# Kernel tuning notes

Measured on AMD Instinct MI355X. Metric: run time of the kernel, lower is better.

Reference implementation:

```python
import jax, jax.numpy as jnp
import numpy as np

N, E, H = 50000, 800000, 4
IN_C, HID_C, OUT_C = 128, 64, 40
NEG_SLOPE_ATT = 0.2   # PyG GATConv default
NEG_SLOPE_ACT = 0.1   # model's LeakyReLU
BN_EPS = 1e-5


def setup_inputs() -> dict:
    key = jax.random.key(0)
    ks = jax.random.split(key, 20)
    x = jax.random.normal(ks[0], (N, IN_C), dtype=jnp.float32)
    adj_m = jax.random.randint(ks[1], (2, E), 0, N, dtype=jnp.int64)
    def glorot(k, shape):
        fan = sum(shape[:2]) if len(shape) == 2 else shape[-1] * 2
        return jax.random.normal(k, shape, dtype=jnp.float32) * (2.0 / fan) ** 0.5
    W0  = glorot(ks[2], (IN_C, H * HID_C))
    as0 = glorot(ks[3], (H, HID_C)); ad0 = glorot(ks[4], (H, HID_C))
    b0  = jnp.zeros((H * HID_C,), jnp.float32)
    W1  = glorot(ks[5], (H * HID_C, H * HID_C))
    as1 = glorot(ks[6], (H, HID_C)); ad1 = glorot(ks[7], (H, HID_C))
    b1  = jnp.zeros((H * HID_C,), jnp.float32)
    # layer 2: 256 -> 40, heads averaged (concat=False)
    W2  = glorot(ks[8], (H * HID_C, H * OUT_C))
    as2 = glorot(ks[9], (H, OUT_C)); ad2 = glorot(ks[10], (H, OUT_C))
    b2  = jnp.zeros((OUT_C,), jnp.float32)
    g0 = jnp.ones((H * HID_C,), jnp.float32); be0 = jnp.zeros((H * HID_C,), jnp.float32)
    g1 = jnp.ones((H * HID_C,), jnp.float32); be1 = jnp.zeros((H * HID_C,), jnp.float32)
    return dict(x=x, adj_m=adj_m, W0=W0, as0=as0, ad0=ad0, b0=b0,
                W1=W1, as1=as1, ad1=ad1, b1=b1, W2=W2, as2=as2, ad2=ad2, b2=b2,
                g0=g0, be0=be0, g1=g1, be1=be1)


def gat_conv(x, src, dst, W, att_src, att_dst, bias, concat):
    n = x.shape[0]
    heads, out_c = att_src.shape
    h = (x @ W).reshape(n, heads, out_c)                       # [N,H,C]
    a_src = jnp.einsum('nhc,hc->nh', h, att_src)               # [N,H]
    a_dst = jnp.einsum('nhc,hc->nh', h, att_dst)
    e = jax.nn.leaky_relu(a_src[src] + a_dst[dst], NEG_SLOPE_ATT)  # [E,H]
    # segment softmax over edges grouped by destination node
    m = jax.ops.segment_max(e, dst, num_segments=n)
    m = jnp.where(jnp.isfinite(m), m, 0.0)
    ee = jnp.exp(e - m[dst])
    s = jax.ops.segment_sum(ee, dst, num_segments=n)
    alpha = ee / (s[dst] + 1e-16)                              # [E,H]
    msg = h[src] * alpha[:, :, None]                           # [E,H,C]
    out = jax.ops.segment_sum(msg, dst, num_segments=n)        # [N,H,C]
    if concat:
        return out.reshape(n, heads * out_c) + bias
    return out.mean(axis=1) + bias


def batch_norm(x, gamma, beta):
    mu = x.mean(axis=0)
    var = x.var(axis=0)
    return (x - mu) * jax.lax.rsqrt(var + BN_EPS) * gamma + beta


def reference(x, adj_m, W0, as0, ad0, b0, W1, as1, ad1, b1,
              W2, as2, ad2, b2, g0, be0, g1, be1):
    n = x.shape[0]
    loop = jnp.arange(n, dtype=adj_m.dtype)
    src = jnp.concatenate([adj_m[0], loop])   # add self-loops (PyG default)
    dst = jnp.concatenate([adj_m[1], loop])
    h = gat_conv(x, src, dst, W0, as0, ad0, b0, True)
    h = jax.nn.leaky_relu(batch_norm(h, g0, be0), NEG_SLOPE_ACT)
    h = gat_conv(h, src, dst, W1, as1, ad1, b1, True)
    h = jax.nn.leaky_relu(batch_norm(h, g1, be1), NEG_SLOPE_ACT)
    h = gat_conv(h, src, dst, W2, as2, ad2, b2, False)
    return jax.nn.log_softmax(h, axis=-1)
```

## Files before the change

kernel.cpp:

```cpp
#include <hip/hip_runtime.h>

#define NNODES 50000
#define NEDGES 800000
#define EPTOT  (NEDGES + NNODES)
#define SCAN_NB ((NNODES + 255) / 256)

typedef unsigned short u16;
typedef unsigned int   u32;
typedef __attribute__((ext_vector_type(8))) short s16x8;
typedef __attribute__((ext_vector_type(4))) float f32x4;

static __device__ __forceinline__ float lrelu(float x, float s) { return x > 0.f ? x : s * x; }
static __device__ __forceinline__ float bf2f(u16 b) { return __uint_as_float((u32)b << 16); }
static __device__ __forceinline__ u16 f2bf(float f) {
  u32 u = __float_as_uint(f);
  u32 r = (u + 0x7FFFu + ((u >> 16) & 1u)) >> 16;
  return (u16)r;
}

__device__ __forceinline__ float wred_max(float v) {
#pragma unroll
  for (int off = 32; off; off >>= 1) v = fmaxf(v, __shfl_xor(v, off));
  return v;
}
__device__ __forceinline__ float wred_sum(float v) {
#pragma unroll
  for (int off = 32; off; off >>= 1) v += __shfl_xor(v, off);
  return v;
}

__global__ void k_hist(const int* __restrict__ adj, int* __restrict__ deg) {
  int i = blockIdx.x * blockDim.x + threadIdx.x;
  if (i >= EPTOT) return;
  int d = (i < NEDGES) ? adj[NEDGES + i] : (i - NEDGES);
  atomicAdd(&deg[d], 1);
}

__global__ __launch_bounds__(256) void k_scan1(const int* __restrict__ deg,
                                               int* __restrict__ part,
                                               int* __restrict__ bsum) {
  __shared__ int sm[256];
  int t = threadIdx.x;
  int i = blockIdx.x * 256 + t;
  int v = (i < NNODES) ? deg[i] : 0;
  sm[t] = v;
  __syncthreads();
#pragma unroll
  for (int off = 1; off < 256; off <<= 1) {
    int u = (t >= off) ? sm[t - off] : 0;
    __syncthreads();
    sm[t] += u;
    __syncthreads();
  }
  if (i < NNODES) part[i] = sm[t] - v;
  if (t == 255) bsum[blockIdx.x] = sm[255];
}

__global__ __launch_bounds__(256) void k_scan2(int* __restrict__ bsum) {
  __shared__ int sm[256];
  int t = threadIdx.x;
  int v = (t < SCAN_NB) ? bsum[t] : 0;
  sm[t] = v;
  __syncthreads();
#pragma unroll
  for (int off = 1; off < 256; off <<= 1) {
    int u = (t >= off) ? sm[t - off] : 0;
    __syncthreads();
    sm[t] += u;
    __syncthreads();
  }
  if (t < SCAN_NB) bsum[t] = sm[t] - v;
}

__global__ __launch_bounds__(256) void k_scan3(const int* __restrict__ part,
                                               const int* __restrict__ bsum,
                                               int* __restrict__ rowptr,
                                               int* __restrict__ fill) {
  int i = blockIdx.x * 256 + threadIdx.x;
  if (i == 0) rowptr[NNODES] = EPTOT;
  if (i >= NNODES) return;
  int r = part[i] + bsum[blockIdx.x];
  rowptr[i] = r;
  fill[i] = r;
}

__global__ void k_fill(const int* __restrict__ adj, int* __restrict__ fill,
                       int* __restrict__ colx) {
  int i = blockIdx.x * blockDim.x + threadIdx.x;
  if (i >= EPTOT) return;
  int s, d;
  if (i < NEDGES) { s = adj[i]; d = adj[NEDGES + i]; }
  else            { s = i - NEDGES; d = s; }
  int pos = atomicAdd(&fill[d], 1);
  colx[pos] = s;
}

__global__ void k_wt(const float* __restrict__ W, u16* __restrict__ Wt, int K, int Nc) {
  int i = blockIdx.x * blockDim.x + threadIdx.x;
  if (i >= K * Nc) return;
  int n = i % Nc, k = i / Nc;
  Wt[(size_t)n * K + k] = f2bf(W[i]);
}

__global__ __launch_bounds__(256) void k_gemm_mfma(const float* __restrict__ A,
                                                   const u16* __restrict__ Wt,
                                                   u16* __restrict__ Cb,
                                                   const float* __restrict__ sc,
                                                   const float* __restrict__ sh,
                                                   int M, int K, int Nc) {
  __shared__ u16 As[128 * 40];
  __shared__ u16 Bs[128 * 40];
  const int tid = threadIdx.x;
  const int lane = tid & 63;
  const int wv = tid >> 6;
  const int wr = (wv >> 1) * 64, wc = (wv & 1) * 64;
  const int lr = lane & 15, lk = (lane >> 4) * 8;
  const int bm = blockIdx.x * 128, bn = blockIdx.y * 128;

  const int row0 = tid >> 2, kc0 = (tid & 3) * 8;
  const int ch1 = tid + 256;
  const int row1 = ch1 >> 2, kc1 = (ch1 & 3) * 8;

  f32x4 acc[4][4];
#pragma unroll
  for (int i = 0; i < 4; ++i)
#pragma unroll
    for (int j = 0; j < 4; ++j) {
      f32x4 z = {0.f, 0.f, 0.f, 0.f};
      acc[i][j] = z;
    }

  for (int k0 = 0; k0 < K; k0 += 32) {
    float4 a00 = {0,0,0,0}, a01 = {0,0,0,0}, a10 = {0,0,0,0}, a11 = {0,0,0,0};
    uint4 bv0 = {0,0,0,0}, bv1 = {0,0,0,0};
    {
      int ga = bm + row0;
      if (ga < M) {
        const float* p = A + (size_t)ga * K + k0 + kc0;
        a00 = *(const float4*)p; a01 = *(const float4*)(p + 4);
      }
      int gb = bn + row0;
      if (gb < Nc) bv0 = *(const uint4*)(Wt + (size_t)gb * K + k0 + kc0);
    }
    {
      int ga = bm + row1;
      if (ga < M) {
        const float* p = A + (size_t)ga * K + k0 + kc1;
        a10 = *(const float4*)p; a11 = *(const float4*)(p + 4);
      }
      int gb = bn + row1;
      if (gb < Nc) bv1 = *(const uint4*)(Wt + (size_t)gb * K + k0 + kc1);
    }
    if (sc) {
      const float* s0p = sc + k0 + kc0; const float* h0p = sh + k0 + kc0;
      a00.x = lrelu(fmaf(a00.x, s0p[0], h0p[0]), 0.1f);
      a00.y = lrelu(fmaf(a00.y, s0p[1], h0p[1]), 0.1f);
      a00.z = lrelu(fmaf(a00.z, s0p[2], h0p[2]), 0.1f);
      a00.w = lrelu(fmaf(a00.w, s0p[3], h0p[3]), 0.1f);
      a01.x = lrelu(fmaf(a01.x, s0p[4], h0p[4]), 0.1f);
      a01.y = lrelu(fmaf(a01.y, s0p[5], h0p[5]), 0.1f);
      a01.z = lrelu(fmaf(a01.z, s0p[6], h0p[6]), 0.1f);
      a01.w = lrelu(fmaf(a01.w, s0p[7], h0p[7]), 0.1f);
      const float* s1p = sc + k0 + kc1; const float* h1p = sh + k0 + kc1;
      a10.x = lrelu(fmaf(a10.x, s1p[0], h1p[0]), 0.1f);
      a10.y = lrelu(fmaf(a10.y, s1p[1], h1p[1]), 0.1f);
      a10.z = lrelu(fmaf(a10.z, s1p[2], h1p[2]), 0.1f);
      a10.w = lrelu(fmaf(a10.w, s1p[3], h1p[3]), 0.1f);
      a11.x = lrelu(fmaf(a11.x, s1p[4], h1p[4]), 0.1f);
      a11.y = lrelu(fmaf(a11.y, s1p[5], h1p[5]), 0.1f);
      a11.z = lrelu(fmaf(a11.z, s1p[6], h1p[6]), 0.1f);
      a11.w = lrelu(fmaf(a11.w, s1p[7], h1p[7]), 0.1f);
    }
    ushort4 h00 = {f2bf(a00.x), f2bf(a00.y), f2bf(a00.z), f2bf(a00.w)};
    ushort4 h01 = {f2bf(a01.x), f2bf(a01.y), f2bf(a01.z), f2bf(a01.w)};
    ushort4 h10 = {f2bf(a10.x), f2bf(a10.y), f2bf(a10.z), f2bf(a10.w)};
    ushort4 h11 = {f2bf(a11.x), f2bf(a11.y), f2bf(a11.z), f2bf(a11.w)};

    __syncthreads();
    *(ushort4*)&As[row0 * 40 + kc0]     = h00;
    *(ushort4*)&As[row0 * 40 + kc0 + 4] = h01;
    *(ushort4*)&As[row1 * 40 + kc1]     = h10;
    *(ushort4*)&As[row1 * 40 + kc1 + 4] = h11;
    *(uint4*)&Bs[row0 * 40 + kc0] = bv0;
    *(uint4*)&Bs[row1 * 40 + kc1] = bv1;
    __syncthreads();

    s16x8 af[4], bfm[4];
#pragma unroll
    for (int mi = 0; mi < 4; ++mi)
      af[mi] = *(const s16x8*)&As[(wr + mi * 16 + lr) * 40 + lk];
#pragma unroll
    for (int ni = 0; ni < 4; ++ni)
      bfm[ni] = *(const s16x8*)&Bs[(wc + ni * 16 + lr) * 40 + lk];
#pragma unroll
    for (int mi = 0; mi < 4; ++mi)
#pragma unroll
      for (int ni = 0; ni < 4; ++ni)
        acc[mi][ni] = __builtin_amdgcn_mfma_f32_16x16x32_bf16(af[mi], bfm[ni], acc[mi][ni], 0, 0, 0);
  }

#pragma unroll
  for (int mi = 0; mi < 4; ++mi) {
    int rowb = bm + wr + mi * 16 + (lane >> 4) * 4;
#pragma unroll
    for (int ni = 0; ni < 4; ++ni) {
      int col = bn + wc + ni * 16 + lr;
      if (col >= Nc) continue;
#pragma unroll
      for (int r = 0; r < 4; ++r) {
        int row = rowb + r;
        if (row < M) Cb[(size_t)row * Nc + col] = f2bf(acc[mi][ni][r]);
      }
    }
  }
}

__global__ __launch_bounds__(256) void k_att_hid(const u16* __restrict__ hb,
                                                 const float* __restrict__ asw,
                                                 const float* __restrict__ adw,
                                                 float* __restrict__ asrc,
                                                 float* __restrict__ adst) {
  int wid = blockIdx.x * 4 + (threadIdx.x >> 6);
  int lane = threadIdx.x & 63;
  if (wid >= NNODES) return;
  const u16* hp = hb + (size_t)wid * 256;
  float v0 = bf2f(hp[lane]), v1 = bf2f(hp[64 + lane]);
  float v2 = bf2f(hp[128 + lane]), v3 = bf2f(hp[192 + lane]);
  float ps0 = v0 * asw[lane],       pd0 = v0 * adw[lane];
  float ps1 = v1 * asw[64 + lane],  pd1 = v1 * adw[64 + lane];
  float ps2 = v2 * asw[128 + lane], pd2 = v2 * adw[128 + lane];
  float ps3 = v3 * asw[192 + lane], pd3 = v3 * adw[192 + lane];
  ps0 = wred_sum(ps0); ps1 = wred_sum(ps1); ps2 = wred_sum(ps2); ps3 = wred_sum(ps3);
  pd0 = wred_sum(pd0); pd1 = wred_sum(pd1); pd2 = wred_sum(pd2); pd3 = wred_sum(pd3);
  if (lane == 0) {
    asrc[wid * 4 + 0] = ps0; asrc[wid * 4 + 1] = ps1;
    asrc[wid * 4 + 2] = ps2; asrc[wid * 4 + 3] = ps3;
    adst[wid * 4 + 0] = pd0; adst[wid * 4 + 1] = pd1;
    adst[wid * 4 + 2] = pd2; adst[wid * 4 + 3] = pd3;
  }
}

__global__ __launch_bounds__(256) void k_att_l2(const u16* __restrict__ hb2,
                                                const float* __restrict__ asw,
                                                const float* __restrict__ adw,
                                                float* __restrict__ asrc,
                                                float* __restrict__ adst) {
  int wid = blockIdx.x * 4 + (threadIdx.x >> 6);
  int lane = threadIdx.x & 63;
  if (wid >= NNODES) return;
  const u16* hp = hb2 + (size_t)wid * 160;
  float ps0 = 0, ps1 = 0, ps2 = 0, ps3 = 0, pd0 = 0, pd1 = 0, pd2 = 0, pd3 = 0;
  if (lane < 40) {
    float v0 = bf2f(hp[lane]), v1 = bf2f(hp[40 + lane]);
    float v2 = bf2f(hp[80 + lane]), v3 = bf2f(hp[120 + lane]);
    ps0 = v0 * asw[lane];       pd0 = v0 * adw[lane];
    ps1 = v1 * asw[40 + lane];  pd1 = v1 * adw[40 + lane];
    ps2 = v2 * asw[80 + lane];  pd2 = v2 * adw[80 + lane];
    ps3 = v3 * asw[120 + lane]; pd3 = v3 * adw[120 + lane];
  }
  ps0 = wred_sum(ps0); ps1 = wred_sum(ps1); ps2 = wred_sum(ps2); ps3 = wred_sum(ps3);
  pd0 = wred_sum(pd0); pd1 = wred_sum(pd1); pd2 = wred_sum(pd2); pd3 = wred_sum(pd3);
  if (lane == 0) {
    asrc[wid * 4 + 0] = ps0; asrc[wid * 4 + 1] = ps1;
    asrc[wid * 4 + 2] = ps2; asrc[wid * 4 + 3] = ps3;
    adst[wid * 4 + 0] = pd0; adst[wid * 4 + 1] = pd1;
    adst[wid * 4 + 2] = pd2; adst[wid * 4 + 3] = pd3;
  }
}

__global__ __launch_bounds__(256) void k_aggr_hid(const u16* __restrict__ hb,
                                                  const float* __restrict__ asrc,
                                                  const float* __restrict__ adst,
                                                  const int* __restrict__ rowptr,
                                                  const int* __restrict__ colx,
                                                  const float* __restrict__ bias,
                                                  u16* __restrict__ ew,
                                                  float* __restrict__ out) {
  int wid = blockIdx.x * 4 + (threadIdx.x >> 6);
  int lane = threadIdx.x & 63;
  if (wid >= NNODES) return;
  int beg = rowptr[wid], end = rowptr[wid + 1];
  float ad0 = adst[wid * 4 + 0], ad1 = adst[wid * 4 + 1];
  float ad2 = adst[wid * 4 + 2], ad3 = adst[wid * 4 + 3];

  float s0 = 0.f, s1 = 0.f, s2 = 0.f, s3 = 0.f;
  for (int i = beg + lane; i < end; i += 64) {
    int s = colx[i];
    const float* ap = asrc + (size_t)s * 4;
    float e0 = expf(lrelu(ap[0] + ad0, 0.2f));
    float e1 = expf(lrelu(ap[1] + ad1, 0.2f));
    float e2 = expf(lrelu(ap[2] + ad2, 0.2f));
    float e3 = expf(lrelu(ap[3] + ad3, 0.2f));
    ushort4 w4 = {f2bf(e0), f2bf(e1), f2bf(e2), f2bf(e3)};
    *(ushort4*)(ew + (size_t)i * 4) = w4;
    s0 += e0; s1 += e1; s2 += e2; s3 += e3;
  }
  s0 = wred_sum(s0); s1 = wred_sum(s1); s2 = wred_sum(s2); s3 = wred_sum(s3);

  int q = lane >> 4;
  float sq = (q == 0) ? s0 : (q == 1) ? s1 : (q == 2) ? s2 : s3;

  float ax = 0.f, ay = 0.f, az = 0.f, aw = 0.f;
  const u16* hbl = hb + lane * 4;
  int i = beg;
  for (; i + 4 <= end; i += 4) {
    int e0 = colx[i], e1 = colx[i + 1], e2 = colx[i + 2], e3 = colx[i + 3];
    float w0 = bf2f(ew[(size_t)i * 4 + q]);
    float w1 = bf2f(ew[(size_t)(i + 1) * 4 + q]);
    float w2 = bf2f(ew[(size_t)(i + 2) * 4 + q]);
    float w3 = bf2f(ew[(size_t)(i + 3) * 4 + q]);
    ushort4 r0 = *(const ushort4*)(hbl + (size_t)e0 * 256);
    ushort4 r1 = *(const ushort4*)(hbl + (size_t)e1 * 256);
    ushort4 r2 = *(const ushort4*)(hbl + (size_t)e2 * 256);
    ushort4 r3 = *(const ushort4*)(hbl + (size_t)e3 * 256);
    ax = fmaf(w0, bf2f(r0.x), ax); ay = fmaf(w0, bf2f(r0.y), ay);
    az = fmaf(w0, bf2f(r0.z), az); aw = fmaf(w0, bf2f(r0.w), aw);
    ax = fmaf(w1, bf2f(r1.x), ax); ay = fmaf(w1, bf2f(r1.y), ay);
    az = fmaf(w1, bf2f(r1.z), az); aw = fmaf(w1, bf2f(r1.w), aw);
    ax = fmaf(w2, bf2f(r2.x), ax); ay = fmaf(w2, bf2f(r2.y), ay);
    az = fmaf(w2, bf2f(r2.z), az); aw = fmaf(w2, bf2f(r2.w), aw);
    ax = fmaf(w3, bf2f(r3.x), ax); ay = fmaf(w3, bf2f(r3.y), ay);
    az = fmaf(w3, bf2f(r3.z), az); aw = fmaf(w3, bf2f(r3.w), aw);
  }
  for (; i < end; ++i) {
    int e0 = colx[i];
    float w0 = bf2f(ew[(size_t)i * 4 + q]);
    ushort4 r0 = *(const ushort4*)(hbl + (size_t)e0 * 256);
    ax = fmaf(w0, bf2f(r0.x), ax); ay = fmaf(w0, bf2f(r0.y), ay);
    az = fmaf(w0, bf2f(r0.z), az); aw = fmaf(w0, bf2f(r0.w), aw);
  }
  float inv = 1.f / (sq + 1e-16f);
  float4 b4 = ((const float4*)bias)[lane];
  float4 o = {fmaf(ax, inv, b4.x), fmaf(ay, inv, b4.y),
              fmaf(az, inv, b4.z), fmaf(aw, inv, b4.w)};
  ((float4*)out)[(size_t)wid * 64 + lane] = o;
}

__global__ __launch_bounds__(256) void k_aggr_l2(const u16* __restrict__ hb2,
                                                 const float* __restrict__ asrc,
                                                 const float* __restrict__ adst,
                                                 const int* __restrict__ rowptr,
                                                 const int* __restrict__ colx,
                                                 const float* __restrict__ b2,
                                                 u16* __restrict__ ew,
                                                 float* __restrict__ out) {
  __shared__ float tile[4][160];
  int wv = threadIdx.x >> 6;
  int wid = blockIdx.x * 4 + wv;
  int lane = threadIdx.x & 63;
  bool valid = (wid < NNODES);
  int beg = 0, end = 0;
  float ad0 = 0, ad1 = 0, ad2 = 0, ad3 = 0;
  if (valid) {
    beg = rowptr[wid]; end = rowptr[wid + 1];
    ad0 = adst[wid * 4 + 0]; ad1 = adst[wid * 4 + 1];
    ad2 = adst[wid * 4 + 2]; ad3 = adst[wid * 4 + 3];
  }
  float s0 = 0.f, s1 = 0.f, s2 = 0.f, s3 = 0.f;
  for (int i = beg + lane; i < end; i += 64) {
    int s = colx[i];
    const float* ap = asrc + (size_t)s * 4;
    float e0 = expf(lrelu(ap[0] + ad0, 0.2f));
    float e1 = expf(lrelu(ap[1] + ad1, 0.2f));
    float e2 = expf(lrelu(ap[2] + ad2, 0.2f));
    float e3 = expf(lrelu(ap[3] + ad3, 0.2f));
    ushort4 w4 = {f2bf(e0), f2bf(e1), f2bf(e2), f2bf(e3)};
    *(ushort4*)(ew + (size_t)i * 4) = w4;
    s0 += e0; s1 += e1; s2 += e2; s3 += e3;
  }
  s0 = wred_sum(s0); s1 = wred_sum(s1); s2 = wred_sum(s2); s3 = wred_sum(s3);

  int q = lane / 10; if (q > 3) q = 3;
  float sq = (q == 0) ? s0 : (q == 1) ? s1 : (q == 2) ? s2 : s3;

  float ax = 0.f, ay = 0.f, az = 0.f, aw = 0.f;
  const u16* hbl = hb2 + lane * 4;
  int i = beg;
  for (; i + 4 <= end; i += 4) {
    int e0 = colx[i], e1 = colx[i + 1], e2 = colx[i + 2], e3 = colx[i + 3];
    float w0 = bf2f(ew[(size_t)i * 4 + q]);
    float w1 = bf2f(ew[(size_t)(i + 1) * 4 + q]);
    float w2 = bf2f(ew[(size_t)(i + 2) * 4 + q]);
    float w3 = bf2f(ew[(size_t)(i + 3) * 4 + q]);
    if (lane < 40) {
      ushort4 r0 = *(const ushort4*)(hbl + (size_t)e0 * 160);
      ushort4 r1 = *(const ushort4*)(hbl + (size_t)e1 * 160);
      ushort4 r2 = *(const ushort4*)(hbl + (size_t)e2 * 160);
      ushort4 r3 = *(const ushort4*)(hbl + (size_t)e3 * 160);
      ax = fmaf(w0, bf2f(r0.x), ax); ay = fmaf(w0, bf2f(r0.y), ay);
      az = fmaf(w0, bf2f(r0.z), az); aw = fmaf(w0, bf2f(r0.w), aw);
      ax = fmaf(w1, bf2f(r1.x), ax); ay = fmaf(w1, bf2f(r1.y), ay);
      az = fmaf(w1, bf2f(r1.z), az); aw = fmaf(w1, bf2f(r1.w), aw);
      ax = fmaf(w2, bf2f(r2.x), ax); ay = fmaf(w2, bf2f(r2.y), ay);
      az = fmaf(w2, bf2f(r2.z), az); aw = fmaf(w2, bf2f(r2.w), aw);
      ax = fmaf(w3, bf2f(r3.x), ax); ay = fmaf(w3, bf2f(r3.y), ay);
      az = fmaf(w3, bf2f(r3.z), az); aw = fmaf(w3, bf2f(r3.w), aw);
    }
  }
  for (; i < end; ++i) {
    int e0 = colx[i];
    float w0 = bf2f(ew[(size_t)i * 4 + q]);
    if (lane < 40) {
      ushort4 r0 = *(const ushort4*)(hbl + (size_t)e0 * 160);
      ax = fmaf(w0, bf2f(r0.x), ax); ay = fmaf(w0, bf2f(r0.y), ay);
      az = fmaf(w0, bf2f(r0.z), az); aw = fmaf(w0, bf2f(r0.w), aw);
    }
  }
  if (valid && lane < 40) {
    float inv = 1.f / (sq + 1e-16f);
    tile[wv][lane * 4 + 0] = ax * inv;
    tile[wv][lane * 4 + 1] = ay * inv;
    tile[wv][lane * 4 + 2] = az * inv;
    tile[wv][lane * 4 + 3] = aw * inv;
  }
  __syncthreads();
  int c = lane;
  float val = -3.0e38f;
  if (valid && c < 40) {
    val = 0.25f * (tile[wv][c] + tile[wv][c + 40] + tile[wv][c + 80] + tile[wv][c + 120]) + b2[c];
  }
  float mv = (valid && c < 40) ? val : -3.0e38f;
  mv = wred_max(mv);
  float ex = (valid && c < 40) ? expf(val - mv) : 0.f;
  ex = wred_sum(ex);
  if (valid && c < 40) out[(size_t)wid * 40 + c] = val - mv - logf(ex);
}

__global__ __launch_bounds__(256) void k_bnstats(const float* __restrict__ x,
                                                 float* __restrict__ stat) {
  int c = threadIdx.x;
  const int rows = (NNODES + gridDim.x - 1) / gridDim.x;
  int r0 = blockIdx.x * rows;
  int r1 = min(NNODES, r0 + rows);
  float s = 0.f, qq = 0.f;
  for (int r = r0; r < r1; ++r) {
    float v = x[(size_t)r * 256 + c];
    s += v;
    qq = fmaf(v, v, qq);
  }
  atomicAdd(&stat[c], s);
  atomicAdd(&stat[256 + c], qq);
}

__global__ void k_bnfin(const float* __restrict__ stat, const float* __restrict__ g,
                        const float* __restrict__ be, float* __restrict__ sc,
                        float* __restrict__ sh) {
  int c = threadIdx.x;
  float mean = stat[c] * (1.0f / NNODES);
  float var = stat[256 + c] * (1.0f / NNODES) - mean * mean;
  float inv = rsqrtf(var + 1e-5f);
  float a = g[c] * inv;
  sc[c] = a;
  sh[c] = be[c] - mean * a;
}

extern "C" void kernel_launch(void* const* d_in, const int* in_sizes, int n_in,
                              void* d_out, int out_size, void* d_ws, size_t ws_size,
                              hipStream_t stream) {
  const float* x   = (const float*)d_in[0];
  const int*   adj = (const int*)d_in[1];
  const float* W0  = (const float*)d_in[2];
  const float* as0 = (const float*)d_in[3];
  const float* ad0 = (const float*)d_in[4];
  const float* b0  = (const float*)d_in[5];
  const float* W1  = (const float*)d_in[6];
  const float* as1 = (const float*)d_in[7];
  const float* ad1 = (const float*)d_in[8];
  const float* b1  = (const float*)d_in[9];
  const float* W2  = (const float*)d_in[10];
  const float* as2 = (const float*)d_in[11];
  const float* ad2 = (const float*)d_in[12];
  const float* b2  = (const float*)d_in[13];
  const float* g0  = (const float*)d_in[14];
  const float* be0 = (const float*)d_in[15];
  const float* g1  = (const float*)d_in[16];
  const float* be1 = (const float*)d_in[17];
  float* out = (float*)d_out;

  float* ws   = (float*)d_ws;
  float* bufA = ws;
  float* asrc = bufA + (size_t)NNODES * 256;
  float* adst = asrc + (size_t)NNODES * 4;
  float* stat = adst + (size_t)NNODES * 4;
  float* bnsc = stat + 512;
  float* bnsh = bnsc + 256;
  u16*   hb   = (u16*)(bnsh + 256);
  u16*   w0t  = hb + (size_t)NNODES * 256;
  u16*   w1t  = w0t + 256 * 128;
  u16*   w2t  = w1t + 256 * 256;
  u16*   ew   = w2t + 160 * 256;
  int* rowptr = (int*)(ew + (size_t)EPTOT * 4);
  int* fill   = rowptr + (NNODES + 1);
  int* colx   = fill + NNODES;
  int* deg    = colx + EPTOT;
  int* part   = deg + NNODES;
  int* bsum   = part + NNODES;

  hipMemsetAsync(deg, 0, NNODES * sizeof(int), stream);
  k_hist<<<(EPTOT + 255) / 256, 256, 0, stream>>>(adj, deg);
  k_scan1<<<SCAN_NB, 256, 0, stream>>>(deg, part, bsum);
  k_scan2<<<1, 256, 0, stream>>>(bsum);
  k_scan3<<<SCAN_NB, 256, 0, stream>>>(part, bsum, rowptr, fill);
  k_fill<<<(EPTOT + 255) / 256, 256, 0, stream>>>(adj, fill, colx);

  k_wt<<<(128 * 256 + 255) / 256, 256, 0, stream>>>(W0, w0t, 128, 256);
  k_wt<<<(256 * 256 + 255) / 256, 256, 0, stream>>>(W1, w1t, 256, 256);
  k_wt<<<(256 * 160 + 255) / 256, 256, 0, stream>>>(W2, w2t, 256, 160);

  dim3 gg2((NNODES + 127) / 128, 2);

  k_gemm_mfma<<<gg2, 256, 0, stream>>>(x, w0t, hb, nullptr, nullptr, NNODES, 128, 256);
  k_att_hid<<<12500, 256, 0, stream>>>(hb, as0, ad0, asrc, adst);
  k_aggr_hid<<<12500, 256, 0, stream>>>(hb, asrc, adst, rowptr, colx, b0, ew, bufA);
  hipMemsetAsync(stat, 0, 512 * sizeof(float), stream);
  k_bnstats<<<400, 256, 0, stream>>>(bufA, stat);
  k_bnfin<<<1, 256, 0, stream>>>(stat, g0, be0, bnsc, bnsh);

  k_gemm_mfma<<<gg2, 256, 0, stream>>>(bufA, w1t, hb, bnsc, bnsh, NNODES, 256, 256);
  k_att_hid<<<12500, 256, 0, stream>>>(hb, as1, ad1, asrc, adst);
  k_aggr_hid<<<12500, 256, 0, stream>>>(hb, asrc, adst, rowptr, colx, b1, ew, bufA);
  hipMemsetAsync(stat, 0, 512 * sizeof(float), stream);
  k_bnstats<<<400, 256, 0, stream>>>(bufA, stat);
  k_bnfin<<<1, 256, 0, stream>>>(stat, g1, be1, bnsc, bnsh);

  k_gemm_mfma<<<gg2, 256, 0, stream>>>(bufA, w2t, hb, bnsc, bnsh, NNODES, 256, 160);
  k_att_l2<<<12500, 256, 0, stream>>>(hb, as2, ad2, asrc, adst);
  k_aggr_l2<<<12500, 256, 0, stream>>>(hb, asrc, adst, rowptr, colx, b2, ew, out);
}
```

Before: 575.1 us.

## Fuse attention logits into GEMM epilogue and store hidden activations as bf16

Folds the per-node attention dot products for the hidden layers into the MFMA GEMM epilogue, reducing each 16-lane group with shuffles and accumulating into zeroed asrc/adst buffers with atomics. This removes a separate pass over the GEMM output. Hidden-layer aggregation outputs are also stored as bf16 instead of fp32, which halves traffic for the batch-norm statistics pass and for the next GEMM's A loads. The cost is extra memsets and atomics, plus some precision loss from bf16 intermediates and from the changed order of atomic summation.

```diff
diff --git a/kernel.cpp b/kernel.cpp
--- a/kernel.cpp
+++ b/kernel.cpp
@@ -102,11 +102,49 @@
   Wt[(size_t)n * K + k] = f2bf(W[i]);
 }
 
-__global__ __launch_bounds__(256) void k_gemm_mfma(const float* __restrict__ A,
+template <int ABF>
+__device__ __forceinline__ void load_a_chunk(const void* __restrict__ Av, int ga, int M,
+                                             int K, int koff, const float* __restrict__ sc,
+                                             const float* __restrict__ sh,
+                                             ushort4& lo, ushort4& hi) {
+  float f[8];
+  if (ABF) {
+    uint4 av = {0, 0, 0, 0};
+    if (ga < M) av = *(const uint4*)((const u16*)Av + (size_t)ga * K + koff);
+    u32 w[4] = {av.x, av.y, av.z, av.w};
+#pragma unroll
+    for (int j = 0; j < 4; ++j) {
+      f[2 * j]     = bf2f((u16)(w[j] & 0xffffu));
+      f[2 * j + 1] = bf2f((u16)(w[j] >> 16));
+    }
+  } else {
+    float4 a0 = {0, 0, 0, 0}, a1 = {0, 0, 0, 0};
+    if (ga < M) {
+      const float* p = (const float*)Av + (size_t)ga * K + koff;
+      a0 = *(const float4*)p;
+      a1 = *(const float4*)(p + 4);
+    }
+    f[0] = a0.x; f[1] = a0.y; f[2] = a0.z; f[3] = a0.w;
+    f[4] = a1.x; f[5] = a1.y; f[6] = a1.z; f[7] = a1.w;
+  }
+  if (sc) {
+#pragma unroll
+    for (int j = 0; j < 8; ++j) f[j] = lrelu(fmaf(f[j], sc[koff + j], sh[koff + j]), 0.1f);
+  }
+  lo = (ushort4){f2bf(f[0]), f2bf(f[1]), f2bf(f[2]), f2bf(f[3])};
+  hi = (ushort4){f2bf(f[4]), f2bf(f[5]), f2bf(f[6]), f2bf(f[7])};
+}
+
+template <int ABF, int ATT>
+__global__ __launch_bounds__(256) void k_gemm_mfma(const void* __restrict__ Av,
                                                    const u16* __restrict__ Wt,
                                                    u16* __restrict__ Cb,
                                                    const float* __restrict__ sc,
                                                    const float* __restrict__ sh,
+                                                   const float* __restrict__ asw,
+                                                   const float* __restrict__ adw,
+                                                   float* __restrict__ asrc,
+                                                   float* __restrict__ adst,
                                                    int M, int K, int Nc) {
   __shared__ u16 As[128 * 40];
   __shared__ u16 Bs[128 * 40];
@@ -131,50 +169,12 @@
     }
 
   for (int k0 = 0; k0 < K; k0 += 32) {
-    float4 a00 = {0,0,0,0}, a01 = {0,0,0,0}, a10 = {0,0,0,0}, a11 = {0,0,0,0};
-    uint4 bv0 = {0,0,0,0}, bv1 = {0,0,0,0};
-    {
-      int ga = bm + row0;
-      if (ga < M) {
-        const float* p = A + (size_t)ga * K + k0 + kc0;
-        a00 = *(const float4*)p; a01 = *(const float4*)(p + 4);
-      }
-      int gb = bn + row0;
-      if (gb < Nc) bv0 = *(const uint4*)(Wt + (size_t)gb * K + k0 + kc0);
-    }
-    {
-      int ga = bm + row1;
-      if (ga < M) {
-        const float* p = A + (size_t)ga * K + k0 + kc1;
-        a10 = *(const float4*)p; a11 = *(const float4*)(p + 4);
-      }
-      int gb = bn + row1;
-      if (gb < Nc) bv1 = *(const uint4*)(Wt + (size_t)gb * K + k0 + kc1);
-    }
-    if (sc) {
-      const float* s0p = sc + k0 + kc0; const float* h0p = sh + k0 + kc0;
-      a00.x = lrelu(fmaf(a00.x, s0p[0], h0p[0]), 0.1f);
-      a00.y = lrelu(fmaf(a00.y, s0p[1], h0p[1]), 0.1f);
-      a00.z = lrelu(fmaf(a00.z, s0p[2], h0p[2]), 0.1f);
-      a00.w = lrelu(fmaf(a00.w, s0p[3], h0p[3]), 0.1f);
-      a01.x = lrelu(fmaf(a01.x, s0p[4], h0p[4]), 0.1f);
-      a01.y = lrelu(fmaf(a01.y, s0p[5], h0p[5]), 0.1f);
-      a01.z = lrelu(fmaf(a01.z, s0p[6], h0p[6]), 0.1f);
-      a01.w = lrelu(fmaf(a01.w, s0p[7], h0p[7]), 0.1f);
-      const float* s1p = sc + k0 + kc1; const float* h1p = sh + k0 + kc1;
-      a10.x = lrelu(fmaf(a10.x, s1p[0], h1p[0]), 0.1f);
-      a10.y = lrelu(fmaf(a10.y, s1p[1], h1p[1]), 0.1f);
-      a10.z = lrelu(fmaf(a10.z, s1p[2], h1p[2]), 0.1f);
-      a10.w = lrelu(fmaf(a10.w, s1p[3], h1p[3]), 0.1f);
-      a11.x = lrelu(fmaf(a11.x, s1p[4], h1p[4]), 0.1f);
-      a11.y = lrelu(fmaf(a11.y, s1p[5], h1p[5]), 0.1f);
-      a11.z = lrelu(fmaf(a11.z, s1p[6], h1p[6]), 0.1f);
-      a11.w = lrelu(fmaf(a11.w, s1p[7], h1p[7]), 0.1f);
-    }
-    ushort4 h00 = {f2bf(a00.x), f2bf(a00.y), f2bf(a00.z), f2bf(a00.w)};
-    ushort4 h01 = {f2bf(a01.x), f2bf(a01.y), f2bf(a01.z), f2bf(a01.w)};
-    ushort4 h10 = {f2bf(a10.x), f2bf(a10.y), f2bf(a10.z), f2bf(a10.w)};
-    ushort4 h11 = {f2bf(a11.x), f2bf(a11.y), f2bf(a11.z), f2bf(a11.w)};
+    ushort4 h00, h01, h10, h11;
+    uint4 bv0 = {0, 0, 0, 0}, bv1 = {0, 0, 0, 0};
+    load_a_chunk<ABF>(Av, bm + row0, M, K, k0 + kc0, sc, sh, h00, h01);
+    load_a_chunk<ABF>(Av, bm + row1, M, K, k0 + kc1, sc, sh, h10, h11);
+    if (bn + row0 < Nc) bv0 = *(const uint4*)(Wt + (size_t)(bn + row0) * K + k0 + kc0);
+    if (bn + row1 < Nc) bv1 = *(const uint4*)(Wt + (size_t)(bn + row1) * K + k0 + kc1);
 
     __syncthreads();
     *(ushort4*)&As[row0 * 40 + kc0]     = h00;
@@ -213,30 +213,33 @@
       }
     }
   }
-}
-
-__global__ __launch_bounds__(256) void k_att_hid(const u16* __restrict__ hb,
-                                                 const float* __restrict__ asw,
-                                                 const float* __restrict__ adw,
-                                                 float* __restrict__ asrc,
-                                                 float* __restrict__ adst) {
-  int wid = blockIdx.x * 4 + (threadIdx.x >> 6);
-  int lane = threadIdx.x & 63;
-  if (wid >= NNODES) return;
-  const u16* hp = hb + (size_t)wid * 256;
-  float v0 = bf2f(hp[lane]), v1 = bf2f(hp[64 + lane]);
-  float v2 = bf2f(hp[128 + lane]), v3 = bf2f(hp[192 + lane]);
-  float ps0 = v0 * asw[lane],       pd0 = v0 * adw[lane];
-  float ps1 = v1 * asw[64 + lane],  pd1 = v1 * adw[64 + lane];
-  float ps2 = v2 * asw[128 + lane], pd2 = v2 * adw[128 + lane];
-  float ps3 = v3 * asw[192 + lane], pd3 = v3 * adw[192 + lane];
-  ps0 = wred_sum(ps0); ps1 = wred_sum(ps1); ps2 = wred_sum(ps2); ps3 = wred_sum(ps3);
-  pd0 = wred_sum(pd0); pd1 = wred_sum(pd1); pd2 = wred_sum(pd2); pd3 = wred_sum(pd3);
-  if (lane == 0) {
-    asrc[wid * 4 + 0] = ps0; asrc[wid * 4 + 1] = ps1;
-    asrc[wid * 4 + 2] = ps2; asrc[wid * 4 + 3] = ps3;
-    adst[wid * 4 + 0] = pd0; adst[wid * 4 + 1] = pd1;
-    adst[wid * 4 + 2] = pd2; adst[wid * 4 + 3] = pd3;
+
+  if (ATT) {
+    int head = (bn + wc) >> 6;
+#pragma unroll
+    for (int mi = 0; mi < 4; ++mi) {
+#pragma unroll
+      for (int r = 0; r < 4; ++r) {
+        int row = bm + wr + mi * 16 + (lane >> 4) * 4 + r;
+        float s = 0.f, d = 0.f;
+#pragma unroll
+        for (int ni = 0; ni < 4; ++ni) {
+          int col = bn + wc + ni * 16 + lr;
+          float v = acc[mi][ni][r];
+          s = fmaf(v, asw[col], s);
+          d = fmaf(v, adw[col], d);
+        }
+#pragma unroll
+        for (int off = 1; off < 16; off <<= 1) {
+          s += __shfl_xor(s, off);
+          d += __shfl_xor(d, off);
+        }
+        if (lr == 0 && row < M) {
+          atomicAdd(&asrc[(size_t)row * 4 + head], s);
+          atomicAdd(&adst[(size_t)row * 4 + head], d);
+        }
+      }
+    }
   }
 }
 
@@ -275,7 +278,7 @@
                                                   const int* __restrict__ colx,
                                                   const float* __restrict__ bias,
                                                   u16* __restrict__ ew,
-                                                  float* __restrict__ out) {
+                                                  u16* __restrict__ outb) {
   int wid = blockIdx.x * 4 + (threadIdx.x >> 6);
   int lane = threadIdx.x & 63;
   if (wid >= NNODES) return;
@@ -331,9 +334,9 @@
   }
   float inv = 1.f / (sq + 1e-16f);
   float4 b4 = ((const float4*)bias)[lane];
-  float4 o = {fmaf(ax, inv, b4.x), fmaf(ay, inv, b4.y),
-              fmaf(az, inv, b4.z), fmaf(aw, inv, b4.w)};
-  ((float4*)out)[(size_t)wid * 64 + lane] = o;
+  ushort4 o = {f2bf(fmaf(ax, inv, b4.x)), f2bf(fmaf(ay, inv, b4.y)),
+               f2bf(fmaf(az, inv, b4.z)), f2bf(fmaf(aw, inv, b4.w))};
+  ((ushort4*)outb)[(size_t)wid * 64 + lane] = o;
 }
 
 __global__ __launch_bounds__(256) void k_aggr_l2(const u16* __restrict__ hb2,
@@ -426,7 +429,7 @@
   if (valid && c < 40) out[(size_t)wid * 40 + c] = val - mv - logf(ex);
 }
 
-__global__ __launch_bounds__(256) void k_bnstats(const float* __restrict__ x,
+__global__ __launch_bounds__(256) void k_bnstats(const u16* __restrict__ x,
                                                  float* __restrict__ stat) {
   int c = threadIdx.x;
   const int rows = (NNODES + gridDim.x - 1) / gridDim.x;
@@ -434,7 +437,7 @@
   int r1 = min(NNODES, r0 + rows);
   float s = 0.f, qq = 0.f;
   for (int r = r0; r < r1; ++r) {
-    float v = x[(size_t)r * 256 + c];
+    float v = bf2f(x[(size_t)r * 256 + c]);
     s += v;
     qq = fmaf(v, v, qq);
   }
@@ -478,14 +481,14 @@
   float* out = (float*)d_out;
 
   float* ws   = (float*)d_ws;
-  float* bufA = ws;
-  float* asrc = bufA + (size_t)NNODES * 256;
+  float* asrc = ws;
   float* adst = asrc + (size_t)NNODES * 4;
   float* stat = adst + (size_t)NNODES * 4;
   float* bnsc = stat + 512;
   float* bnsh = bnsc + 256;
   u16*   hb   = (u16*)(bnsh + 256);
-  u16*   w0t  = hb + (size_t)NNODES * 256;
+  u16*   hbo  = hb + (size_t)NNODES * 256;
+  u16*   w0t  = hbo + (size_t)NNODES * 256;
   u16*   w1t  = w0t + 256 * 128;
   u16*   w2t  = w1t + 256 * 256;
   u16*   ew   = w2t + 160 * 256;
@@ -509,21 +512,25 @@
 
   dim3 gg2((NNODES + 127) / 128, 2);
 
-  k_gemm_mfma<<<gg2, 256, 0, stream>>>(x, w0t, hb, nullptr, nullptr, NNODES, 128, 256);
-  k_att_hid<<<12500, 256, 0, stream>>>(hb, as0, ad0, asrc, adst);
-  k_aggr_hid<<<12500, 256, 0, stream>>>(hb, asrc, adst, rowptr, colx, b0, ew, bufA);
+  hipMemsetAsync(asrc, 0, (size_t)NNODES * 8 * sizeof(float), stream);
+  k_gemm_mfma<0, 1><<<gg2, 256, 0, stream>>>(x, w0t, hb, nullptr, nullptr,
+                                             as0, ad0, asrc, adst, NNODES, 128, 256);
+  k_aggr_hid<<<12500, 256, 0, stream>>>(hb, asrc, adst, rowptr, colx, b0, ew, hbo);
   hipMemsetAsync(stat, 0, 512 * sizeof(float), stream);
-  k_bnstats<<<400, 256, 0, stream>>>(bufA, stat);
+  k_bnstats<<<400, 256, 0, stream>>>(hbo, stat);
   k_bnfin<<<1, 256, 0, stream>>>(stat, g0, be0, bnsc, bnsh);
 
-  k_gemm_mfma<<<gg2, 256, 0, stream>>>(bufA, w1t, hb, bnsc, bnsh, NNODES, 256, 256);
-  k_att_hid<<<12500, 256, 0, stream>>>(hb, as1, ad1, asrc, adst);
-  k_aggr_hid<<<12500, 256, 0, stream>>>(hb, asrc, adst, rowptr, colx, b1, ew, bufA);
+  hipMemsetAsync(asrc, 0, (size_t)NNODES * 8 * sizeof(float), stream);
+  k_gemm_mfma<1, 1><<<gg2, 256, 0, stream>>>(hbo, w1t, hb, bnsc, bnsh,
+                                             as1, ad1, asrc, adst, NNODES, 256, 256);
+  k_aggr_hid<<<12500, 256, 0, stream>>>(hb, asrc, adst, rowptr, colx, b1, ew, hbo);
   hipMemsetAsync(stat, 0, 512 * sizeof(float), stream);
-  k_bnstats<<<400, 256, 0, stream>>>(bufA, stat);
+  k_bnstats<<<400, 256, 0, stream>>>(hbo, stat);
   k_bnfin<<<1, 256, 0, stream>>>(stat, g1, be1, bnsc, bnsh);
 
-  k_gemm_mfma<<<gg2, 256, 0, stream>>>(bufA, w2t, hb, bnsc, bnsh, NNODES, 256, 160);
+  k_gemm_mfma<1, 0><<<gg2, 256, 0, stream>>>(hbo, w2t, hb, bnsc, bnsh,
+                                             nullptr, nullptr, nullptr, nullptr,
+                                             NNODES, 256, 160);
   k_att_l2<<<12500, 256, 0, stream>>>(hb, as2, ad2, asrc, adst);
   k_aggr_l2<<<12500, 256, 0, stream>>>(hb, asrc, adst, rowptr, colx, b2, ew, out);
 }
```

After: 565.8 us. No clear change (-1.6%).
